# Kernel tuning notes

Measured on AMD Instinct MI355X. Metric: run time of the kernel, lower is better.

Reference implementation:

```python
import jax, jax.numpy as jnp
import numpy as np

DIM = 512
N_HEADS = 8
HEAD_DIM = DIM // N_HEADS


def setup_inputs() -> dict:
    key = jax.random.key(0)
    ks = jax.random.split(key, 11)
    B, S = 2, 2048
    s = 1.0 / np.sqrt(DIM)
    return {
        "q": jax.random.normal(ks[0], (B, S, DIM), jnp.float32),
        "k": jax.random.normal(ks[1], (B, S, DIM), jnp.float32),
        "v": jax.random.normal(ks[2], (B, S, DIM), jnp.float32),
        "Wq": jax.random.normal(ks[3], (DIM, DIM), jnp.float32) * s,
        "bq": jnp.zeros((DIM,), jnp.float32),
        "Wk": jax.random.normal(ks[4], (DIM, DIM), jnp.float32) * s,
        "bk": jnp.zeros((DIM,), jnp.float32),
        "Wv": jax.random.normal(ks[5], (DIM, DIM), jnp.float32) * s,
        "bv": jnp.zeros((DIM,), jnp.float32),
        "Wo": jax.random.normal(ks[6], (DIM, DIM), jnp.float32) * s,
        "bo": jnp.zeros((DIM,), jnp.float32),
    }


def reference(q, k, v, Wq, bq, Wk, bk, Wv, bv, Wo, bo):
    B, S, _ = q.shape
    # projections; split into heads: [B, H, S, Dh]
    def proj(x, W, b):
        y = x @ W.T + b
        return y.reshape(B, -1, N_HEADS, HEAD_DIM).transpose(0, 2, 1, 3)

    qh = proj(q, Wq, bq)
    kh = proj(k, Wk, bk)
    vh = proj(v, Wv, bv)
    scores = jnp.einsum("bhsd,bhtd->bhst", qh, kh) / np.sqrt(HEAD_DIM)
    attn = jax.nn.softmax(scores, axis=-1)  # dropout = identity in eval
    ctx = jnp.einsum("bhst,bhtd->bhsd", attn, vh)
    ctx = ctx.transpose(0, 2, 1, 3).reshape(B, S, DIM)
    out = ctx @ Wo.T + bo
    return out, attn
```

## Files before the change

### kernel.cpp

```cpp
#include <hip/hip_runtime.h>
#include <math.h>

#define DIM 512
#define NH 8
#define HD 64
#define SS 2048
#define NB 2

typedef __bf16 bf16;
typedef __attribute__((ext_vector_type(8))) __bf16 bf16x8;
typedef __attribute__((ext_vector_type(4))) __bf16 bf16x4;
typedef __attribute__((ext_vector_type(2))) __bf16 bf16x2;
typedef __attribute__((ext_vector_type(4))) float f32x4;

__device__ inline bf16x8 cvt8(const float* s) {
  bf16x8 o;
#pragma unroll
  for (int i = 0; i < 8; ++i) o[i] = (bf16)s[i];
  return o;
}

__device__ inline void bar_lds_only() {
  asm volatile("s_waitcnt lgkmcnt(0)" ::: "memory");
  __builtin_amdgcn_s_barrier();
}

__global__ __launch_bounds__(256) void qkv_proj_kernel(
    const float* __restrict__ xq, const float* __restrict__ xk, const float* __restrict__ xv,
    const float* __restrict__ Wq, const float* __restrict__ bq,
    const float* __restrict__ Wk, const float* __restrict__ bk,
    const float* __restrict__ Wv, const float* __restrict__ bv,
    bf16* __restrict__ qh, bf16* __restrict__ kh, bf16* __restrict__ vh)
{
  const int which = blockIdx.z;
  const float* A    = (which == 0) ? xq : (which == 1) ? xk : xv;
  const float* W    = (which == 0) ? Wq : (which == 1) ? Wk : Wv;
  const float* bias = (which == 0) ? bq : (which == 1) ? bk : bv;
  bf16* out         = (which == 0) ? qh : (which == 1) ? kh : vh;
  const float oscale = (which == 0) ? 0.125f : 1.0f;

  __shared__ bf16 As[128][72];
  __shared__ bf16 Bs[64][72];

  const int m0 = blockIdx.x * 128;
  const int n0 = blockIdx.y * 64;
  const int tid = threadIdx.x;
  const int w = tid >> 6, l = tid & 63;
  const int l16 = l & 15, lg = l >> 4;
  const int wm = w >> 1, wn = w & 1;

  f32x4 acc[4][2];
#pragma unroll
  for (int mf = 0; mf < 4; ++mf)
#pragma unroll
    for (int nf = 0; nf < 2; ++nf) acc[mf][nf] = (f32x4){0.f, 0.f, 0.f, 0.f};

  for (int k0 = 0; k0 < DIM; k0 += 64) {
    __syncthreads();
    {
      const int r = tid >> 1, hf = (tid & 1) * 32;
      const float* src = &A[(size_t)(m0 + r) * DIM + k0 + hf];
      bf16* dst = &As[r][hf];
#pragma unroll
      for (int i = 0; i < 4; ++i) ((bf16x8*)dst)[i] = cvt8(src + i * 8);
    }
    if (tid < 128) {
      const int r = tid >> 1, hf = (tid & 1) * 32;
      const float* src = &W[(size_t)(n0 + r) * DIM + k0 + hf];
      bf16* dst = &Bs[r][hf];
#pragma unroll
      for (int i = 0; i < 4; ++i) ((bf16x8*)dst)[i] = cvt8(src + i * 8);
    }
    __syncthreads();

#pragma unroll
    for (int kk = 0; kk < 2; ++kk) {
      bf16x8 bfr[2];
      bfr[0] = *(const bf16x8*)&Bs[wn * 32 + l16][kk * 32 + lg * 8];
      bfr[1] = *(const bf16x8*)&Bs[wn * 32 + 16 + l16][kk * 32 + lg * 8];
#pragma unroll
      for (int mf = 0; mf < 4; ++mf) {
        const bf16x8 af = *(const bf16x8*)&As[wm * 64 + mf * 16 + l16][kk * 32 + lg * 8];
        acc[mf][0] = __builtin_amdgcn_mfma_f32_16x16x32_bf16(af, bfr[0], acc[mf][0], 0, 0, 0);
        acc[mf][1] = __builtin_amdgcn_mfma_f32_16x16x32_bf16(af, bfr[1], acc[mf][1], 0, 0, 0);
      }
    }
  }

  const int h = blockIdx.y;
#pragma unroll
  for (int mf = 0; mf < 4; ++mf) {
#pragma unroll
    for (int nf = 0; nf < 2; ++nf) {
      const int d = wn * 32 + nf * 16 + l16;
#pragma unroll
      for (int ri = 0; ri < 4; ++ri) {
        const int row = m0 + wm * 64 + mf * 16 + lg * 4 + ri;
        const int b = row >> 11, s = row & 2047;
        out[((size_t)(b * NH + h) * SS + s) * HD + d] =
            (bf16)((acc[mf][nf][ri] + bias[n0 + d]) * oscale);
      }
    }
  }
}

__global__ __launch_bounds__(256, 8) void sums_kernel(
    const bf16* __restrict__ qh, const bf16* __restrict__ kh,
    float* __restrict__ partial)
{
  __shared__ __align__(16) bf16 Ks[2][64][72];

  const int lin  = blockIdx.x;
  const int work = (lin & 7) * 128 + (lin >> 3);
  const int half = work & 1;
  const int qb   = (work >> 1) & 31;
  const int bh   = work >> 6;
  const int q0   = qb * 64;

  const int tid = threadIdx.x;
  const int w   = tid >> 6;
  const int l   = tid & 63;
  const int l16 = l & 15;
  const int lg  = l >> 4;

  const bf16* qp = qh + (size_t)bh * SS * HD;
  const bf16* kp = kh + ((size_t)bh * SS + half * 1024) * HD;

  const int ks_r = tid >> 2;
  const int ks_c = (tid & 3) * 16;
  const bf16* kstage = &kp[(size_t)ks_r * HD + ks_c];

  const int qrow = q0 + w * 16 + l16;
  const bf16x8 qf0 = *(const bf16x8*)&qp[(size_t)qrow * HD + lg * 8];
  const bf16x8 qf1 = *(const bf16x8*)&qp[(size_t)qrow * HD + 32 + lg * 8];

  {
    ((bf16x8*)&Ks[0][ks_r][ks_c])[0] = ((const bf16x8*)kstage)[0];
    ((bf16x8*)&Ks[0][ks_r][ks_c])[1] = ((const bf16x8*)kstage)[1];
  }
  bar_lds_only();

  float lsum = 0.f;
  int cur = 0;
  for (int tt = 0; tt < 1024; tt += 64) {
    bf16x8 kr0, kr1;
    const bool has_next = (tt + 64) < 1024;
    if (has_next) {
      const bf16* src = kstage + (size_t)(tt + 64) * HD;
      kr0 = ((const bf16x8*)src)[0];
      kr1 = ((const bf16x8*)src)[1];
    }

#pragma unroll
    for (int n = 0; n < 4; ++n) {
      const bf16x8 kf0 = *(const bf16x8*)&Ks[cur][n * 16 + l16][lg * 8];
      const bf16x8 kf1 = *(const bf16x8*)&Ks[cur][n * 16 + l16][32 + lg * 8];
      f32x4 a = {0.f, 0.f, 0.f, 0.f};
      a = __builtin_amdgcn_mfma_f32_16x16x32_bf16(kf0, qf0, a, 0, 0, 0);
      a = __builtin_amdgcn_mfma_f32_16x16x32_bf16(kf1, qf1, a, 0, 0, 0);
#pragma unroll
      for (int reg = 0; reg < 4; ++reg) lsum += __expf(a[reg]);
    }
    if (has_next) {
      ((bf16x8*)&Ks[cur ^ 1][ks_r][ks_c])[0] = kr0;
      ((bf16x8*)&Ks[cur ^ 1][ks_r][ks_c])[1] = kr1;
    }
    bar_lds_only();
    cur ^= 1;
  }

  lsum += __shfl_xor(lsum, 16);
  lsum += __shfl_xor(lsum, 32);
  if (lg == 0) partial[(((size_t)bh * SS) + q0 + w * 16 + l16) * 2 + half] = lsum;
}

__global__ __launch_bounds__(512, 4) void attn_kernel(
    const bf16* __restrict__ qh, const bf16* __restrict__ kh, const bf16* __restrict__ vh,
    const float* __restrict__ partial,
    float* __restrict__ attn, bf16* __restrict__ ctx)
{
  __shared__ __align__(16) bf16 Ks[2][64][72];
  __shared__ __align__(16) bf16 Vt[2][64][72];
  __shared__ __align__(16) bf16 Ps[8][16][128];

  const int lin  = blockIdx.x;
  const int work = (lin & 7) * 64 + (lin >> 3);
  const int bh = work >> 5;
  const int q0 = (work & 31) * 64;

  const int tid = threadIdx.x;
  const int w   = tid >> 6;
  const int wq  = w >> 1;
  const int wt  = w & 1;
  const int l   = tid & 63;
  const int l16 = l & 15;
  const int lg  = l >> 4;

  const bf16* qp = qh + (size_t)bh * SS * HD;
  const bf16* kp = kh + (size_t)bh * SS * HD;
  const bf16* vp = vh + (size_t)bh * SS * HD;

  const int ks_wt = tid >> 8;
  const int ks_r  = (tid >> 2) & 63;
  const int ks_c  = (tid & 3) * 16;
  const int vs_wt = tid >> 8;
  const int vs_rc = (tid >> 3) & 31;
  const int vs_dc = tid & 7;

  const bf16* kstage = &kp[(size_t)(ks_wt * 1024 + ks_r) * HD + ks_c];
  const bf16* vstage = &vp[(size_t)(vs_wt * 1024 + vs_rc * 2) * HD + vs_dc * 8];
  bf16* ks_dst = &Ks[ks_wt][ks_r][ks_c];
  const int vcolbase = (((vs_rc >> 2) ^ vs_dc) << 3) | ((vs_rc & 3) << 1);

  const int qrow = q0 + wq * 16 + l16;
  const bf16x8 qf0 = *(const bf16x8*)&qp[(size_t)qrow * HD + lg * 8];
  const bf16x8 qf1 = *(const bf16x8*)&qp[(size_t)qrow * HD + 32 + lg * 8];

  const int tbase = wt * 1024;

  const float inv_l = 1.f / (partial[((size_t)bh * SS + qrow) * 2 + 0] +
                             partial[((size_t)bh * SS + qrow) * 2 + 1]);

  f32x4 accC[4];
#pragma unroll
  for (int dt = 0; dt < 4; ++dt) accC[dt] = (f32x4){0.f, 0.f, 0.f, 0.f};

  float* arow = attn + ((size_t)(bh * SS + q0 + wq * 16 + l16)) * SS + tbase;
  char* psbase = (char*)&Ps[w][0][0] + l16 * 256;

  {
    ((bf16x8*)ks_dst)[0] = ((const bf16x8*)kstage)[0];
    ((bf16x8*)ks_dst)[1] = ((const bf16x8*)kstage)[1];
    const bf16x8 v0 = *(const bf16x8*)vstage;
    const bf16x8 v1 = *(const bf16x8*)(vstage + HD);
#pragma unroll
    for (int j = 0; j < 8; ++j) {
      *(bf16x2*)&Vt[vs_wt][vs_dc * 8 + j][vcolbase] = (bf16x2){v0[j], v1[j]};
    }
  }

  for (int tt = 0; tt < 1024; tt += 64) {
    bf16x8 kr0, kr1, vr0, vr1;
    const bool has_next = (tt + 64) < 1024;
    if (has_next) {
      const bf16* ksrc = kstage + (size_t)(tt + 64) * HD;
      kr0 = ((const bf16x8*)ksrc)[0];
      kr1 = ((const bf16x8*)ksrc)[1];
      const bf16* vsrc = vstage + (size_t)(tt + 64) * HD;
      vr0 = *(const bf16x8*)vsrc;
      vr1 = *(const bf16x8*)(vsrc + HD);
    }
    bar_lds_only();

#pragma unroll
    for (int n = 0; n < 4; ++n) {
      const bf16x8 kf0 = *(const bf16x8*)&Ks[wt][n * 16 + l16][lg * 8];
      const bf16x8 kf1 = *(const bf16x8*)&Ks[wt][n * 16 + l16][32 + lg * 8];
      f32x4 a = {0.f, 0.f, 0.f, 0.f};
      a = __builtin_amdgcn_mfma_f32_16x16x32_bf16(kf0, qf0, a, 0, 0, 0);
      a = __builtin_amdgcn_mfma_f32_16x16x32_bf16(kf1, qf1, a, 0, 0, 0);

      float4 pv;
      bf16x4 p4;
#pragma unroll
      for (int reg = 0; reg < 4; ++reg) {
        const float p = __expf(a[reg]) * inv_l;
        ((float*)&pv)[reg] = p;
        p4[reg] = (bf16)p;
      }
      *(float4*)&arow[tt + n * 16 + lg * 4] = pv;
      *(bf16x4*)(psbase + ((((n << 1) | (lg >> 1)) ^ (l16 & 7)) << 4) + ((lg & 1) << 3)) = p4;
    }

#pragma unroll
    for (int ts = 0; ts < 2; ++ts) {
      const bf16x8 pa = *(const bf16x8*)(psbase + ((((ts << 2) | lg) ^ (l16 & 7)) << 4));
#pragma unroll
      for (int dt = 0; dt < 4; ++dt) {
        const int vcol = (((ts * 4 + lg) ^ ((dt * 2 + (l16 >> 3)) & 7)) << 3);
        const bf16x8 vb = *(const bf16x8*)&Vt[wt][dt * 16 + l16][vcol];
        accC[dt] = __builtin_amdgcn_mfma_f32_16x16x32_bf16(vb, pa, accC[dt], 0, 0, 0);
      }
    }
    bar_lds_only();
    if (has_next) {
      ((bf16x8*)ks_dst)[0] = kr0;
      ((bf16x8*)ks_dst)[1] = kr1;
#pragma unroll
      for (int j = 0; j < 8; ++j) {
        *(bf16x2*)&Vt[vs_wt][vs_dc * 8 + j][vcolbase] = (bf16x2){vr0[j], vr1[j]};
      }
    }
  }

  __syncthreads();
  float* cred = (float*)&Ks[0][0][0];
  if (wt == 1) {
#pragma unroll
    for (int dt = 0; dt < 4; ++dt)
      *(f32x4*)&cred[(wq * 16 + l16) * 68 + dt * 16 + lg * 4] = accC[dt];
  }
  __syncthreads();
  if (wt == 0) {
    const int b = bh >> 3, h = bh & 7;
    bf16* crow = ctx + ((size_t)b * SS + q0 + wq * 16 + l16) * DIM + h * HD;
#pragma unroll
    for (int dt = 0; dt < 4; ++dt) {
      const f32x4 o = *(const f32x4*)&cred[(wq * 16 + l16) * 68 + dt * 16 + lg * 4];
      bf16x4 cb;
#pragma unroll
      for (int reg = 0; reg < 4; ++reg) cb[reg] = (bf16)(accC[dt][reg] + o[reg]);
      *(bf16x4*)&crow[dt * 16 + lg * 4] = cb;
    }
  }
}

__global__ __launch_bounds__(256) void out_proj_kernel(
    const bf16* __restrict__ ctx, const float* __restrict__ Wo, const float* __restrict__ bo,
    float* __restrict__ out)
{
  __shared__ bf16 As[128][72];
  __shared__ bf16 Bs[64][72];

  const int m0 = blockIdx.x * 128;
  const int n0 = blockIdx.y * 64;
  const int tid = threadIdx.x;
  const int w = tid >> 6, l = tid & 63;
  const int l16 = l & 15, lg = l >> 4;
  const int wm = w >> 1, wn = w & 1;

  f32x4 acc[4][2];
#pragma unroll
  for (int mf = 0; mf < 4; ++mf)
#pragma unroll
    for (int nf = 0; nf < 2; ++nf) acc[mf][nf] = (f32x4){0.f, 0.f, 0.f, 0.f};

  for (int k0 = 0; k0 < DIM; k0 += 64) {
    __syncthreads();
    {
      const int r = tid >> 1, hf = (tid & 1) * 32;
      const bf16* src = &ctx[(size_t)(m0 + r) * DIM + k0 + hf];
      bf16* dst = &As[r][hf];
#pragma unroll
      for (int i = 0; i < 4; ++i) ((bf16x8*)dst)[i] = ((const bf16x8*)src)[i];
    }
    if (tid < 128) {
      const int r = tid >> 1, hf = (tid & 1) * 32;
      const float* src = &Wo[(size_t)(n0 + r) * DIM + k0 + hf];
      bf16* dst = &Bs[r][hf];
#pragma unroll
      for (int i = 0; i < 4; ++i) ((bf16x8*)dst)[i] = cvt8(src + i * 8);
    }
    __syncthreads();

#pragma unroll
    for (int kk = 0; kk < 2; ++kk) {
      bf16x8 bfr[2];
      bfr[0] = *(const bf16x8*)&Bs[wn * 32 + l16][kk * 32 + lg * 8];
      bfr[1] = *(const bf16x8*)&Bs[wn * 32 + 16 + l16][kk * 32 + lg * 8];
#pragma unroll
      for (int mf = 0; mf < 4; ++mf) {
        const bf16x8 af = *(const bf16x8*)&As[wm * 64 + mf * 16 + l16][kk * 32 + lg * 8];
        acc[mf][0] = __builtin_amdgcn_mfma_f32_16x16x32_bf16(af, bfr[0], acc[mf][0], 0, 0, 0);
        acc[mf][1] = __builtin_amdgcn_mfma_f32_16x16x32_bf16(af, bfr[1], acc[mf][1], 0, 0, 0);
      }
    }
  }

#pragma unroll
  for (int mf = 0; mf < 4; ++mf) {
#pragma unroll
    for (int nf = 0; nf < 2; ++nf) {
      const int c = n0 + wn * 32 + nf * 16 + l16;
#pragma unroll
      for (int ri = 0; ri < 4; ++ri) {
        const int row = m0 + wm * 64 + mf * 16 + lg * 4 + ri;
        out[(size_t)row * DIM + c] = acc[mf][nf][ri] + bo[c];
      }
    }
  }
}

extern "C" void kernel_launch(void* const* d_in, const int* in_sizes, int n_in,
                              void* d_out, int out_size, void* d_ws, size_t ws_size,
                              hipStream_t stream) {
  const float* q  = (const float*)d_in[0];
  const float* k  = (const float*)d_in[1];
  const float* v  = (const float*)d_in[2];
  const float* Wq = (const float*)d_in[3];
  const float* bq = (const float*)d_in[4];
  const float* Wk = (const float*)d_in[5];
  const float* bk = (const float*)d_in[6];
  const float* Wv = (const float*)d_in[7];
  const float* bv = (const float*)d_in[8];
  const float* Wo = (const float*)d_in[9];
  const float* bo = (const float*)d_in[10];

  float* out0 = (float*)d_out;
  float* attn = out0 + (size_t)NB * SS * DIM;

  const size_t HSZ = (size_t)NB * NH * SS * HD;
  bf16* qh  = (bf16*)d_ws;
  bf16* kh  = qh + HSZ;
  bf16* vh  = kh + HSZ;
  bf16* ctx = vh + HSZ;
  float* partial = (float*)(ctx + (size_t)NB * SS * DIM);

  dim3 g1(NB * SS / 128, DIM / 64, 3);
  qkv_proj_kernel<<<g1, 256, 0, stream>>>(q, k, v, Wq, bq, Wk, bk, Wv, bv, qh, kh, vh);

  dim3 g2a(NB * NH * (SS / 64) * 2);
  sums_kernel<<<g2a, 256, 0, stream>>>(qh, kh, partial);

  dim3 g2(SS / 64 * NB * NH);
  attn_kernel<<<g2, 512, 0, stream>>>(qh, kh, vh, partial, attn, ctx);

  dim3 g3(NB * SS / 128, DIM / 64);
  out_proj_kernel<<<g3, 256, 0, stream>>>(ctx, Wo, bo, out0);
}
```

Measured before the change: 139.5 us.

## Split attention key range into four blocks and reduce partial contexts in out-proj

```diff
diff --git a/kernel.cpp b/kernel.cpp
--- a/kernel.cpp
+++ b/kernel.cpp
@@ -174,24 +174,25 @@
   if (lg == 0) partial[(((size_t)bh * SS) + q0 + w * 16 + l16) * 2 + half] = lsum;
 }
 
-__global__ __launch_bounds__(512, 4) void attn_kernel(
+__global__ __launch_bounds__(256, 4) void attn_kernel(
     const bf16* __restrict__ qh, const bf16* __restrict__ kh, const bf16* __restrict__ vh,
     const float* __restrict__ partial,
-    float* __restrict__ attn, bf16* __restrict__ ctx)
+    float* __restrict__ attn, bf16* __restrict__ ctxp)
 {
-  __shared__ __align__(16) bf16 Ks[2][64][72];
-  __shared__ __align__(16) bf16 Vt[2][64][72];
-  __shared__ __align__(16) bf16 Ps[8][16][128];
+  __shared__ __align__(16) bf16 Ks[64][72];
+  __shared__ __align__(16) bf16 Vt[64][72];
+  __shared__ __align__(16) bf16 Ps[4][16][80];
 
   const int lin  = blockIdx.x;
-  const int work = (lin & 7) * 64 + (lin >> 3);
-  const int bh = work >> 5;
-  const int q0 = (work & 31) * 64;
+  const int work = (lin & 7) * 256 + (lin >> 3);
+  const int tq   = work & 3;
+  const int qb   = (work >> 2) & 31;
+  const int bh   = work >> 7;
+  const int q0   = qb * 64;
+  const int t0b  = tq * 512;
 
   const int tid = threadIdx.x;
   const int w   = tid >> 6;
-  const int wq  = w >> 1;
-  const int wt  = w & 1;
   const int l   = tid & 63;
   const int l16 = l & 15;
   const int lg  = l >> 4;
@@ -200,24 +201,20 @@
   const bf16* kp = kh + (size_t)bh * SS * HD;
   const bf16* vp = vh + (size_t)bh * SS * HD;
 
-  const int ks_wt = tid >> 8;
-  const int ks_r  = (tid >> 2) & 63;
+  const int ks_r  = tid >> 2;
   const int ks_c  = (tid & 3) * 16;
-  const int vs_wt = tid >> 8;
   const int vs_rc = (tid >> 3) & 31;
   const int vs_dc = tid & 7;
 
-  const bf16* kstage = &kp[(size_t)(ks_wt * 1024 + ks_r) * HD + ks_c];
-  const bf16* vstage = &vp[(size_t)(vs_wt * 1024 + vs_rc * 2) * HD + vs_dc * 8];
-  bf16* ks_dst = &Ks[ks_wt][ks_r][ks_c];
+  const bf16* kstage = &kp[(size_t)(t0b + ks_r) * HD + ks_c];
+  const bf16* vstage = &vp[(size_t)(t0b + vs_rc * 2) * HD + vs_dc * 8];
+  bf16* ks_dst = &Ks[ks_r][ks_c];
   const int vcolbase = (((vs_rc >> 2) ^ vs_dc) << 3) | ((vs_rc & 3) << 1);
 
-  const int qrow = q0 + wq * 16 + l16;
+  const int qrow = q0 + w * 16 + l16;
   const bf16x8 qf0 = *(const bf16x8*)&qp[(size_t)qrow * HD + lg * 8];
   const bf16x8 qf1 = *(const bf16x8*)&qp[(size_t)qrow * HD + 32 + lg * 8];
 
-  const int tbase = wt * 1024;
-
   const float inv_l = 1.f / (partial[((size_t)bh * SS + qrow) * 2 + 0] +
                              partial[((size_t)bh * SS + qrow) * 2 + 1]);
 
@@ -225,8 +222,8 @@
 #pragma unroll
   for (int dt = 0; dt < 4; ++dt) accC[dt] = (f32x4){0.f, 0.f, 0.f, 0.f};
 
-  float* arow = attn + ((size_t)(bh * SS + q0 + wq * 16 + l16)) * SS + tbase;
-  char* psbase = (char*)&Ps[w][0][0] + l16 * 256;
+  float* arow = attn + ((size_t)(bh * SS + qrow)) * SS + t0b;
+  char* psbase = (char*)&Ps[w][0][0] + l16 * 160;
 
   {
     ((bf16x8*)ks_dst)[0] = ((const bf16x8*)kstage)[0];
@@ -235,13 +232,13 @@
     const bf16x8 v1 = *(const bf16x8*)(vstage + HD);
 #pragma unroll
     for (int j = 0; j < 8; ++j) {
-      *(bf16x2*)&Vt[vs_wt][vs_dc * 8 + j][vcolbase] = (bf16x2){v0[j], v1[j]};
-    }
-  }
-
-  for (int tt = 0; tt < 1024; tt += 64) {
+      *(bf16x2*)&Vt[vs_dc * 8 + j][vcolbase] = (bf16x2){v0[j], v1[j]};
+    }
+  }
+
+  for (int tt = 0; tt < 512; tt += 64) {
     bf16x8 kr0, kr1, vr0, vr1;
-    const bool has_next = (tt + 64) < 1024;
+    const bool has_next = (tt + 64) < 512;
     if (has_next) {
       const bf16* ksrc = kstage + (size_t)(tt + 64) * HD;
       kr0 = ((const bf16x8*)ksrc)[0];
@@ -254,8 +251,8 @@
 
 #pragma unroll
     for (int n = 0; n < 4; ++n) {
-      const bf16x8 kf0 = *(const bf16x8*)&Ks[wt][n * 16 + l16][lg * 8];
-      const bf16x8 kf1 = *(const bf16x8*)&Ks[wt][n * 16 + l16][32 + lg * 8];
+      const bf16x8 kf0 = *(const bf16x8*)&Ks[n * 16 + l16][lg * 8];
+      const bf16x8 kf1 = *(const bf16x8*)&Ks[n * 16 + l16][32 + lg * 8];
       f32x4 a = {0.f, 0.f, 0.f, 0.f};
       a = __builtin_amdgcn_mfma_f32_16x16x32_bf16(kf0, qf0, a, 0, 0, 0);
       a = __builtin_amdgcn_mfma_f32_16x16x32_bf16(kf1, qf1, a, 0, 0, 0);
@@ -278,7 +275,7 @@
 #pragma unroll
       for (int dt = 0; dt < 4; ++dt) {
         const int vcol = (((ts * 4 + lg) ^ ((dt * 2 + (l16 >> 3)) & 7)) << 3);
-        const bf16x8 vb = *(const bf16x8*)&Vt[wt][dt * 16 + l16][vcol];
+        const bf16x8 vb = *(const bf16x8*)&Vt[dt * 16 + l16][vcol];
         accC[dt] = __builtin_amdgcn_mfma_f32_16x16x32_bf16(vb, pa, accC[dt], 0, 0, 0);
       }
     }
@@ -288,39 +285,31 @@
       ((bf16x8*)ks_dst)[1] = kr1;
 #pragma unroll
       for (int j = 0; j < 8; ++j) {
-        *(bf16x2*)&Vt[vs_wt][vs_dc * 8 + j][vcolbase] = (bf16x2){vr0[j], vr1[j]};
-      }
-    }
-  }
-
-  __syncthreads();
-  float* cred = (float*)&Ks[0][0][0];
-  if (wt == 1) {
-#pragma unroll
-    for (int dt = 0; dt < 4; ++dt)
-      *(f32x4*)&cred[(wq * 16 + l16) * 68 + dt * 16 + lg * 4] = accC[dt];
-  }
-  __syncthreads();
-  if (wt == 0) {
-    const int b = bh >> 3, h = bh & 7;
-    bf16* crow = ctx + ((size_t)b * SS + q0 + wq * 16 + l16) * DIM + h * HD;
-#pragma unroll
-    for (int dt = 0; dt < 4; ++dt) {
-      const f32x4 o = *(const f32x4*)&cred[(wq * 16 + l16) * 68 + dt * 16 + lg * 4];
-      bf16x4 cb;
-#pragma unroll
-      for (int reg = 0; reg < 4; ++reg) cb[reg] = (bf16)(accC[dt][reg] + o[reg]);
-      *(bf16x4*)&crow[dt * 16 + lg * 4] = cb;
-    }
+        *(bf16x2*)&Vt[vs_dc * 8 + j][vcolbase] = (bf16x2){vr0[j], vr1[j]};
+      }
+    }
+  }
+
+  const int b = bh >> 3, h = bh & 7;
+  bf16* crow = ctxp + (size_t)tq * NB * SS * DIM +
+               ((size_t)b * SS + qrow) * DIM + h * HD;
+#pragma unroll
+  for (int dt = 0; dt < 4; ++dt) {
+    bf16x4 cb;
+#pragma unroll
+    for (int reg = 0; reg < 4; ++reg) cb[reg] = (bf16)accC[dt][reg];
+    *(bf16x4*)&crow[dt * 16 + lg * 4] = cb;
   }
 }
 
 __global__ __launch_bounds__(256) void out_proj_kernel(
-    const bf16* __restrict__ ctx, const float* __restrict__ Wo, const float* __restrict__ bo,
+    const bf16* __restrict__ ctxp, const float* __restrict__ Wo, const float* __restrict__ bo,
     float* __restrict__ out)
 {
   __shared__ bf16 As[128][72];
   __shared__ bf16 Bs[64][72];
+
+  const size_t CH = (size_t)NB * SS * DIM;
 
   const int m0 = blockIdx.x * 128;
   const int n0 = blockIdx.y * 64;
@@ -339,10 +328,20 @@
     __syncthreads();
     {
       const int r = tid >> 1, hf = (tid & 1) * 32;
-      const bf16* src = &ctx[(size_t)(m0 + r) * DIM + k0 + hf];
+      const bf16* s0 = &ctxp[(size_t)(m0 + r) * DIM + k0 + hf];
       bf16* dst = &As[r][hf];
 #pragma unroll
-      for (int i = 0; i < 4; ++i) ((bf16x8*)dst)[i] = ((const bf16x8*)src)[i];
+      for (int i = 0; i < 4; ++i) {
+        const bf16x8 a0 = ((const bf16x8*)s0)[i];
+        const bf16x8 a1 = ((const bf16x8*)(s0 + CH))[i];
+        const bf16x8 a2 = ((const bf16x8*)(s0 + 2 * CH))[i];
+        const bf16x8 a3 = ((const bf16x8*)(s0 + 3 * CH))[i];
+        bf16x8 o;
+#pragma unroll
+        for (int j = 0; j < 8; ++j)
+          o[j] = (bf16)((float)a0[j] + (float)a1[j] + (float)a2[j] + (float)a3[j]);
+        ((bf16x8*)dst)[i] = o;
+      }
     }
     if (tid < 128) {
       const int r = tid >> 1, hf = (tid & 1) * 32;
@@ -400,11 +399,11 @@
   float* attn = out0 + (size_t)NB * SS * DIM;
 
   const size_t HSZ = (size_t)NB * NH * SS * HD;
-  bf16* qh  = (bf16*)d_ws;
-  bf16* kh  = qh + HSZ;
-  bf16* vh  = kh + HSZ;
-  bf16* ctx = vh + HSZ;
-  float* partial = (float*)(ctx + (size_t)NB * SS * DIM);
+  bf16* qh   = (bf16*)d_ws;
+  bf16* kh   = qh + HSZ;
+  bf16* vh   = kh + HSZ;
+  bf16* ctxp = vh + HSZ;
+  float* partial = (float*)(ctxp + 4 * (size_t)NB * SS * DIM);
 
   dim3 g1(NB * SS / 128, DIM / 64, 3);
   qkv_proj_kernel<<<g1, 256, 0, stream>>>(q, k, v, Wq, bq, Wk, bk, Wv, bv, qh, kh, vh);
@@ -412,9 +411,9 @@
   dim3 g2a(NB * NH * (SS / 64) * 2);
   sums_kernel<<<g2a, 256, 0, stream>>>(qh, kh, partial);
 
-  dim3 g2(SS / 64 * NB * NH);
-  attn_kernel<<<g2, 512, 0, stream>>>(qh, kh, vh, partial, attn, ctx);
+  dim3 g2(NB * NH * (SS / 64) * 4);
+  attn_kernel<<<g2, 256, 0, stream>>>(qh, kh, vh, partial, attn, ctxp);
 
   dim3 g3(NB * SS / 128, DIM / 64);
-  out_proj_kernel<<<g3, 256, 0, stream>>>(ctx, Wo, bo, out0);
-}
+  out_proj_kernel<<<g3, 256, 0, stream>>>(ctxp, Wo, bo, out0);
+}
```

New measurement: 150.9 us. 8.2% more time.
